# Performance work log

Measured on AMD Instinct MI355X. Metric: run time of the kernel, lower is better.

Reference implementation:

```python
import jax, jax.numpy as jnp
import numpy as np

H = 2048
Q_RANK = 256
SCALE = float(np.sqrt(Q_RANK))


def setup_inputs() -> dict:
    key = jax.random.key(0)
    k_x, k_s, k_a, k_o, k_b = jax.random.split(key, 5)
    B, L = 4, 4096
    x = jax.random.normal(k_x, (B, L, H), dtype=jnp.float32)
    # nn.Linear(H, q_rank, bias=False): weight [q_rank, H]; y = x @ W.T -> store transposed [H, q_rank]
    Ws = jax.random.normal(k_s, (H, Q_RANK), dtype=jnp.float32) / np.sqrt(H)
    Wa = jax.random.normal(k_a, (H, Q_RANK), dtype=jnp.float32) / np.sqrt(H)
    Wo = jax.random.normal(k_o, (H, H), dtype=jnp.float32) / np.sqrt(H)
    bo = jax.random.normal(k_b, (H,), dtype=jnp.float32) * 0.01
    return {"x": x, "Ws": Ws, "Wa": Wa, "Wo": Wo, "bo": bo}


def reference(x, Ws, Wa, Wo, bo):
    # x: [B, L, H]
    B, L, _ = x.shape
    state = jnp.einsum('blh,hr->blr', x, Ws)   # [B, L, r]
    action = jnp.einsum('blh,hr->blr', x, Wa)  # [B, L, r]
    q_values = jnp.einsum('bir,bjr->bij', state, action) / SCALE  # [B, L, L]
    # causal mask: position i attends to j <= i
    causal = jnp.tril(jnp.ones((L, L), dtype=bool))
    q_values = jnp.where(causal, q_values, -jnp.inf)
    weights = jax.nn.softmax(q_values, axis=-1)  # [B, L, L]
    out = jnp.einsum('bij,bjh->bih', weights, x)  # weights @ x (x acts as V)
    return jnp.einsum('bih,ho->bio', out, Wo.T) + bo  # out_proj: y = out @ Wo_lin.T; Wo stored as [H,H] input-major
```

## Files before the change

### kernel.cpp

```cpp
#include <hip/hip_runtime.h>
#include <hip/hip_bf16.h>
#include <cstdint>
#include <cstddef>
#include <cmath>

typedef __bf16 bf16_t;
typedef __bf16 bf16x8 __attribute__((ext_vector_type(8)));
typedef __bf16 bf16x4v __attribute__((ext_vector_type(4)));
typedef float f32x4 __attribute__((ext_vector_type(4)));

#define B_SZ 4
#define L_SZ 4096
#define H_SZ 2048
#define R_SZ 256
#define EXP_SC 0.090168440f
#define E2_ELEMS 8912896L
#define E2_BYTES 17825792L

#define GLDS16(gaddr, laddr)                                                    \
  __builtin_amdgcn_global_load_lds(                                             \
      (const __attribute__((address_space(1))) void*)(gaddr),                   \
      (__attribute__((address_space(3))) void*)(laddr), 16, 0, 0)

__device__ __forceinline__ f32x4 mfma16(bf16x8 a, bf16x8 b, f32x4 c) {
  return __builtin_amdgcn_mfma_f32_16x16x32_bf16(a, b, c, 0, 0, 0);
}

__device__ __forceinline__ float rsum16(float v) {
  v += __shfl_xor(v, 1, 16);
  v += __shfl_xor(v, 2, 16);
  v += __shfl_xor(v, 4, 16);
  v += __shfl_xor(v, 8, 16);
  return v;
}

__global__ void conv_kernel(const float* __restrict__ x, const float* __restrict__ Ws,
                            const float* __restrict__ Wa, const float* __restrict__ Wo,
                            bf16_t* __restrict__ xb, bf16_t* __restrict__ Wst,
                            bf16_t* __restrict__ Wat, bf16_t* __restrict__ Wob,
                            float* __restrict__ lsum) {
  const int bid = blockIdx.x;
  const int t = threadIdx.x;
  if (bid < 1280) {
    const int tid = bid * 256 + t;
    const int stride = 1280 * 256;
    const int n4 = B_SZ * L_SZ * H_SZ / 4;
    for (int i = tid; i < n4; i += stride) {
      float4 v = reinterpret_cast<const float4*>(x)[i];
      bf16x4v o;
      o[0] = (bf16_t)v.x; o[1] = (bf16_t)v.y; o[2] = (bf16_t)v.z; o[3] = (bf16_t)v.w;
      reinterpret_cast<bf16x4v*>(xb)[i] = o;
    }
  } else if (bid < 1920) {
    const int tid = (bid - 1280) * 256 + t;
    const int stride = 640 * 256;
    for (int idx = tid; idx < H_SZ * H_SZ / 4; idx += stride) {
      float4 v = reinterpret_cast<const float4*>(Wo)[idx];
      bf16x4v o;
      o[0] = (bf16_t)v.x; o[1] = (bf16_t)v.y; o[2] = (bf16_t)v.z; o[3] = (bf16_t)v.w;
      reinterpret_cast<bf16x4v*>(Wob)[idx] = o;
    }
  } else if (bid < 2040) {
    __shared__ float tile[32][33];
    const int j = t & 31;
    const int i4 = t >> 5;
    for (int tt = bid - 1920; tt < 1024; tt += 120) {
      const int mat = tt >> 9;
      const int ti = tt & 511;
      const int h0 = (ti >> 3) * 32;
      const int r0 = (ti & 7) * 32;
      const float* src = mat ? Wa : Ws;
      bf16_t* dst = mat ? Wat : Wst;
      __syncthreads();
#pragma unroll
      for (int p = 0; p < 4; ++p) {
        const int ii = p * 8 + i4;
        tile[ii][j] = src[(long)(h0 + ii) * R_SZ + r0 + j];
      }
      __syncthreads();
#pragma unroll
      for (int p = 0; p < 4; ++p) {
        const int rr = p * 8 + i4;
        dst[(long)(r0 + rr) * H_SZ + h0 + j] = (bf16_t)tile[j][rr];
      }
    }
  } else {
    const int tid = (bid - 2040) * 256 + t;
    const int stride = 8 * 256;
    for (int idx = tid; idx < B_SZ * L_SZ; idx += stride) lsum[idx] = 0.0f;
  }
}


#define G8_STG(P, REGION, BUFOFF, HALF)                                        \
  GLDS16((P)[0], lds + (REGION) + (BUFOFF) + (HALF)*16384 + ldst0);            \
  GLDS16((P)[1], lds + (REGION) + (BUFOFF) + (HALF)*16384 + ldst1);            \
  (P)[0] += 128; (P)[1] += 128;

#define G8_LDA(MH, BO) {                                                       \
  const char* ap_ = lds + (BO) + (MH)*16384;                                   \
  fa[0][0] = *(const bf16x8*)(ap_ + aOff0);                                    \
  fa[0][1] = *(const bf16x8*)(ap_ + aOff1);                                    \
  fa[1][0] = *(const bf16x8*)(ap_ + 4096 + aOff0);                             \
  fa[1][1] = *(const bf16x8*)(ap_ + 4096 + aOff1);                             \
  fa[2][0] = *(const bf16x8*)(ap_ + 8192 + aOff0);                             \
  fa[2][1] = *(const bf16x8*)(ap_ + 8192 + aOff1);                             \
  fa[3][0] = *(const bf16x8*)(ap_ + 12288 + aOff0);                            \
  fa[3][1] = *(const bf16x8*)(ap_ + 12288 + aOff1); }

#define G8_LDB(NH, BO) {                                                       \
  const char* bp_ = lds + 65536 + (BO) + (NH)*16384;                           \
  fb[NH][0][0] = *(const bf16x8*)(bp_ + bOff0);                                \
  fb[NH][0][1] = *(const bf16x8*)(bp_ + bOff1);                                \
  fb[NH][1][0] = *(const bf16x8*)(bp_ + 8192 + bOff0);                         \
  fb[NH][1][1] = *(const bf16x8*)(bp_ + 8192 + bOff1); }

#define G8_MM1(AM, AN, MF, NH, J)                                              \
  acc[AM][AN] = mfma16(fa[MF][1], fb[NH][J][1],                                \
                 mfma16(fa[MF][0], fb[NH][J][0], acc[AM][AN]))

#define G8_MM(MH, NH)                                                          \
  G8_MM1((MH)*4+0, (NH)*2+0, 0, NH, 0); G8_MM1((MH)*4+0, (NH)*2+1, 0, NH, 1); \
  G8_MM1((MH)*4+1, (NH)*2+0, 1, NH, 0); G8_MM1((MH)*4+1, (NH)*2+1, 1, NH, 1); \
  G8_MM1((MH)*4+2, (NH)*2+0, 2, NH, 0); G8_MM1((MH)*4+2, (NH)*2+1, 2, NH, 1); \
  G8_MM1((MH)*4+3, (NH)*2+0, 3, NH, 0); G8_MM1((MH)*4+3, (NH)*2+1, 3, NH, 1)

template <bool FULLN>
__device__ __forceinline__ void gemm8_core(
    const char* Ag, const char* Bg, long aRowB, long bRowB, int NT,
    char* lds, f32x4 (&acc)[8][4])
{
  const int t = threadIdx.x;
  const int l = t & 63;
  const int wid = t >> 6;
  const int wr = wid >> 2;
  const int wc = wid & 3;
  const int l15 = l & 15;
  const int l4 = l >> 4;
  const int swzm = (l15 & 7) << 4;
  const int aOff0 = (wr * 16 + l15) * 128 + ((l4 * 16) ^ swzm);
  const int aOff1 = (wr * 16 + l15) * 128 + ((64 + l4 * 16) ^ swzm);
  const int bOff0 = (wc * 16 + l15) * 128 + ((l4 * 16) ^ swzm);
  const int bOff1 = (wc * 16 + l15) * 128 + ((64 + l4 * 16) ^ swzm);
  const int d0 = t * 16, d1 = t * 16 + 8192;
  const int r0 = d0 >> 7, r1 = d1 >> 7;
  const int s0 = (d0 & 127) ^ ((r0 & 7) << 4);
  const int s1 = (d1 & 127) ^ ((r1 & 7) << 4);
  const char* pA0[2] = { Ag + (long)r0 * aRowB + s0, Ag + (long)r1 * aRowB + s1 };
  const char* pA1[2] = { Ag + (long)(128 + r0) * aRowB + s0, Ag + (long)(128 + r1) * aRowB + s1 };
  const char* pB0[2] = { Bg + (long)r0 * bRowB + s0, Bg + (long)r1 * bRowB + s1 };
  const char* pB1[2] = { Bg + (long)(128 + r0) * bRowB + s0, Bg + (long)(128 + r1) * bRowB + s1 };
  const int ldst0 = wid * 1024, ldst1 = wid * 1024 + 8192;
  bf16x8 fa[4][2], fb[2][2][2];

  G8_STG(pA0, 0, 0, 0);
  G8_STG(pB0, 65536, 0, 0);
  G8_STG(pA1, 0, 0, 1);
  if constexpr (FULLN) { G8_STG(pB1, 65536, 0, 1); }
  G8_STG(pA0, 0, 32768, 0);
  G8_STG(pB0, 65536, 32768, 0);
  asm volatile("s_waitcnt vmcnt(4)" ::: "memory");
  __builtin_amdgcn_sched_barrier(0);
  __builtin_amdgcn_s_barrier();

  int bufOff = 0;
  for (int T = 0; T < NT; ++T) {
    const int ob = bufOff ^ 32768;
    const bool stg1 = (T < NT - 1);
    const bool stg2 = (T < NT - 2);
    G8_LDA(0, bufOff);
    G8_LDB(0, bufOff);
    if constexpr (FULLN) { G8_LDB(1, bufOff); }
    if (stg1) {
      G8_STG(pA1, 0, ob, 1);
      if constexpr (FULLN) { G8_STG(pB1, 65536, ob, 1); }
    }
    __builtin_amdgcn_s_setprio(1);
    G8_MM(0, 0);
    if constexpr (FULLN) { G8_MM(0, 1); }
    __builtin_amdgcn_s_setprio(0);
    G8_LDA(1, bufOff);
    asm volatile("s_waitcnt lgkmcnt(8)" ::: "memory");
    __builtin_amdgcn_sched_barrier(0);
    __builtin_amdgcn_s_barrier();
    if (stg2) {
      G8_STG(pA0, 0, bufOff, 0);
      G8_STG(pB0, 65536, bufOff, 0);
    }
    asm volatile("s_waitcnt lgkmcnt(0)" ::: "memory");
    __builtin_amdgcn_s_setprio(1);
    G8_MM(1, 0);
    if constexpr (FULLN) { G8_MM(1, 1); }
    __builtin_amdgcn_s_setprio(0);
    if (stg2) {
      asm volatile("s_waitcnt vmcnt(4)" ::: "memory");
    } else if (stg1) {
      asm volatile("s_waitcnt vmcnt(0)" ::: "memory");
    }
    __builtin_amdgcn_sched_barrier(0);
    __builtin_amdgcn_s_barrier();
    bufOff ^= 32768;
  }
}

__global__ __launch_bounds__(512) void vq8_kernel(
    const bf16_t* __restrict__ Wob, const bf16_t* __restrict__ xb, bf16_t* __restrict__ VT,
    const bf16_t* __restrict__ Wst, const bf16_t* __restrict__ Wat,
    bf16_t* __restrict__ Qb, bf16_t* __restrict__ Kb)
{
  extern __shared__ char lds[];
  const int f = blockIdx.x;
  const int t = threadIdx.x, l = t & 63, wid = t >> 6;
  const int wr = wid >> 2, wc = wid & 3, l15 = l & 15, l4 = l >> 4;
  f32x4 acc[8][4] = {};
  if (f < 512) {
    const int lg = (f & 7) * 64 + (f >> 3);
    const int xo = lg & 7;
    const int yj = (lg >> 3) & 15;
    const int b  = lg >> 7;
    const long mBase = (long)xo * 256;
    const long nBase = (long)yj * 256;
    gemm8_core<true>((const char*)Wob + mBase * (H_SZ * 2),
                     (const char*)xb + ((long)b * L_SZ + nBase) * (H_SZ * 2),
                     H_SZ * 2, H_SZ * 2, H_SZ / 64, lds, acc);
    bf16_t* Cp = VT + (long)b * H_SZ * L_SZ;
#pragma unroll
    for (int am = 0; am < 8; ++am) {
#pragma unroll
      for (int an = 0; an < 4; ++an) {
        const long row = mBase + wr * 16 + am * 32 + l4 * 4;
        const long col = nBase + wc * 16 + an * 64 + l15;
#pragma unroll
        for (int r = 0; r < 4; ++r)
          Cp[(row + r) * L_SZ + col] = (bf16_t)acc[am][an][r];
      }
    }
  } else {
    const int qf = f - 512;
    const int lg = (qf & 7) * 32 + (qf >> 3);
    const int m = lg & 63;
    const int n = (lg >> 6) & 1;
    const int proj = lg >> 7;
    const long mBase = (long)m * 256;
    const long nBase = (long)n * 128;
    const bf16_t* W = proj ? Wat : Wst;
    bf16_t* Cp = proj ? Kb : Qb;
    gemm8_core<false>((const char*)xb + mBase * (H_SZ * 2),
                      (const char*)W + nBase * (H_SZ * 2),
                      H_SZ * 2, H_SZ * 2, H_SZ / 64, lds, acc);
#pragma unroll
    for (int am = 0; am < 8; ++am) {
#pragma unroll
      for (int an = 0; an < 2; ++an) {
        const long row = mBase + wr * 16 + am * 32 + l4 * 4;
        const long col = nBase + wc * 16 + an * 64 + l15;
#pragma unroll
        for (int r = 0; r < 4; ++r)
          Cp[(row + r) * R_SZ + col] = (bf16_t)acc[am][an][r];
      }
    }
  }
}

__global__ __launch_bounds__(512) void ep8_kernel(
    const bf16_t* __restrict__ Qb, const bf16_t* __restrict__ Kb,
    bf16_t* __restrict__ E, float* __restrict__ lsum)
{
  extern __shared__ char lds[];
  const int f = blockIdx.x;
  const int lg = (f & 7) * 68 + (f >> 3);
  const int b = lg / 136;
  const int t136 = lg - b * 136;
  int P = (int)((sqrtf((float)(8 * t136 + 1)) - 1.0f) * 0.5f);
  while ((P + 1) * (P + 2) / 2 <= t136) ++P;
  while (P * (P + 1) / 2 > t136) --P;
  const int Jp = t136 - P * (P + 1) / 2;

  f32x4 acc[8][4] = {};
  gemm8_core<true>((const char*)Qb + ((long)b * L_SZ + P * 256) * (R_SZ * 2),
                   (const char*)Kb + ((long)b * L_SZ + Jp * 256) * (R_SZ * 2),
                   R_SZ * 2, R_SZ * 2, R_SZ / 64, lds, acc);
  const int t = threadIdx.x, l = t & 63, wid = t >> 6;
  const int wr = wid >> 2, wc = wid & 3, l15 = l & 15, l4 = l >> 4;
  bf16_t* Ep = E + (long)b * E2_ELEMS + 32768L * P * (P + 1);
  const long ldaE = (long)(P + 1) * 256;
  float* lp = lsum + (long)b * L_SZ + P * 256;
  const bool diag = (Jp == P);
#pragma unroll
  for (int am = 0; am < 8; ++am) {
    const int rowi = wr * 16 + am * 32 + l4 * 4;
#pragma unroll
    for (int r = 0; r < 4; ++r) {
      float s = 0.0f;
#pragma unroll
      for (int an = 0; an < 4; ++an) {
        const int coli = wc * 16 + an * 64 + l15;
        float p = exp2f(acc[am][an][r] * EXP_SC);
        if (diag && coli > rowi + r) p = 0.0f;
        Ep[(long)(rowi + r) * ldaE + Jp * 256 + coli] = (bf16_t)p;
        s += p;
      }
      s = rsum16(s);
      if (l15 == 0) atomicAdd(lp + rowi + r, s);
    }
  }
}

__global__ __launch_bounds__(512) void pv8_kernel(
    const bf16_t* __restrict__ E, const bf16_t* __restrict__ VT,
    const float* __restrict__ lsum, const float* __restrict__ bo,
    float* __restrict__ out)
{
  extern __shared__ char lds[];
  const int f = blockIdx.x;
  const int lg = (f & 7) * 32 + (f >> 3);
  const int yj = lg & 7;
  const int pr = (lg >> 3) & 7;
  const int b  = lg >> 6;
  const int nBase = yj * 256;
  const int t = threadIdx.x, l = t & 63, wid = t >> 6;
  const int wr = wid >> 2, wc = wid & 3, l15 = l & 15, l4 = l >> 4;

#pragma unroll
  for (int s = 0; s < 2; ++s) {
    const int mt = s ? pr : (15 - pr);
    f32x4 acc[8][4] = {};
    const char* Ag = (const char*)E + (long)b * E2_BYTES + 65536L * mt * (mt + 1);
    const char* Bg = (const char*)VT + ((long)b * H_SZ + nBase) * (L_SZ * 2);
    gemm8_core<true>(Ag, Bg, (long)(mt + 1) * 512, L_SZ * 2, (mt + 1) * 4, lds, acc);
#pragma unroll
    for (int am = 0; am < 8; ++am) {
      const long rowG = (long)b * L_SZ + mt * 256 + wr * 16 + am * 32 + l4 * 4;
      float linv[4];
#pragma unroll
      for (int r = 0; r < 4; ++r) linv[r] = 1.0f / lsum[rowG + r];
#pragma unroll
      for (int an = 0; an < 4; ++an) {
        const int col = nBase + wc * 16 + an * 64 + l15;
        const float bias = bo[col];
#pragma unroll
        for (int r = 0; r < 4; ++r)
          out[(rowG + r) * H_SZ + col] = acc[am][an][r] * linv[r] + bias;
      }
    }
  }
}

extern "C" void kernel_launch(void* const* d_in, const int* in_sizes, int n_in,
                              void* d_out, int out_size, void* d_ws, size_t ws_size,
                              hipStream_t stream) {
  const float* x  = (const float*)d_in[0];
  const float* Ws = (const float*)d_in[1];
  const float* Wa = (const float*)d_in[2];
  const float* Wo = (const float*)d_in[3];
  const float* bo = (const float*)d_in[4];
  float* out = (float*)d_out;

  char* ws = (char*)d_ws;
  bf16_t* xb  = (bf16_t*)(ws + 0);
  bf16_t* Wst = (bf16_t*)(ws + 67108864);
  bf16_t* Wat = (bf16_t*)(ws + 68157440);
  bf16_t* Wob = (bf16_t*)(ws + 69206016);
  bf16_t* Qb  = (bf16_t*)(ws + 77594624);
  bf16_t* Kb  = (bf16_t*)(ws + 85983232);
  bf16_t* VT  = (bf16_t*)(ws + 94371840);
  float*  lsum = (float*)(ws + 161480704);
  bf16_t* E   = (bf16_t*)(ws + 0);

  hipFuncSetAttribute((const void*)vq8_kernel, hipFuncAttributeMaxDynamicSharedMemorySize, 131072);
  hipFuncSetAttribute((const void*)ep8_kernel, hipFuncAttributeMaxDynamicSharedMemorySize, 131072);
  hipFuncSetAttribute((const void*)pv8_kernel, hipFuncAttributeMaxDynamicSharedMemorySize, 131072);

  conv_kernel<<<dim3(2048), dim3(256), 0, stream>>>(x, Ws, Wa, Wo, xb, Wst, Wat, Wob, lsum);
  vq8_kernel<<<dim3(768), dim3(512), 131072, stream>>>(Wob, xb, VT, Wst, Wat, Qb, Kb);
  ep8_kernel<<<dim3(544), dim3(512), 131072, stream>>>(Qb, Kb, E, lsum);
  pv8_kernel<<<dim3(256), dim3(512), 131072, stream>>>(E, VT, lsum, bo, out);
}
```

Baseline: 367.5 us.

## Triple-buffer the B operand in LDS to prefetch two k-tiles ahead

The shared GEMM core now keeps the B tile in a ring of six 16KB LDS slots (three stages) instead of a double buffer, and issues B global-to-LDS loads two iterations ahead. The second B half (FULLN) is no longer staged just one iteration before use. vmcnt wait counts are adjusted to match, and the dynamic LDS allocation grows to 160KB for all three kernels. The aim is to hide more global-load latency for B, at the cost of using the full LDS budget and adding slot-rotation arithmetic.

Result: no change. 366.6 us (-0.2%).

```diff
diff --git a/kernel.cpp b/kernel.cpp
--- a/kernel.cpp
+++ b/kernel.cpp
@@ -16,6 +16,7 @@
 #define EXP_SC 0.090168440f
 #define E2_ELEMS 8912896L
 #define E2_BYTES 17825792L
+#define LDS_BYTES 163840
 
 #define GLDS16(gaddr, laddr)                                                    \
   __builtin_amdgcn_global_load_lds(                                             \
@@ -97,6 +98,11 @@
   GLDS16((P)[1], lds + (REGION) + (BUFOFF) + (HALF)*16384 + ldst1);            \
   (P)[0] += 128; (P)[1] += 128;
 
+#define GB_STG(P, S)                                                           \
+  GLDS16((P)[0], lds + 65536 + (S)*16384 + ldst0);                             \
+  GLDS16((P)[1], lds + 65536 + (S)*16384 + ldst1);                             \
+  (P)[0] += 128; (P)[1] += 128;
+
 #define G8_LDA(MH, BO) {                                                       \
   const char* ap_ = lds + (BO) + (MH)*16384;                                   \
   fa[0][0] = *(const bf16x8*)(ap_ + aOff0);                                    \
@@ -108,8 +114,8 @@
   fa[3][0] = *(const bf16x8*)(ap_ + 12288 + aOff0);                            \
   fa[3][1] = *(const bf16x8*)(ap_ + 12288 + aOff1); }
 
-#define G8_LDB(NH, BO) {                                                       \
-  const char* bp_ = lds + 65536 + (BO) + (NH)*16384;                           \
+#define G8_LDB(NH, S) {                                                        \
+  const char* bp_ = lds + 65536 + ((S) + (NH)) * 16384;                        \
   fb[NH][0][0] = *(const bf16x8*)(bp_ + bOff0);                                \
   fb[NH][0][1] = *(const bf16x8*)(bp_ + bOff1);                                \
   fb[NH][1][0] = *(const bf16x8*)(bp_ + 8192 + bOff0);                         \
@@ -154,26 +160,34 @@
   bf16x8 fa[4][2], fb[2][2][2];
 
   G8_STG(pA0, 0, 0, 0);
-  G8_STG(pB0, 65536, 0, 0);
   G8_STG(pA1, 0, 0, 1);
-  if constexpr (FULLN) { G8_STG(pB1, 65536, 0, 1); }
+  GB_STG(pB0, 0);
+  if constexpr (FULLN) { GB_STG(pB1, 1); }
   G8_STG(pA0, 0, 32768, 0);
-  G8_STG(pB0, 65536, 32768, 0);
-  asm volatile("s_waitcnt vmcnt(4)" ::: "memory");
+  GB_STG(pB0, 2);
+  if constexpr (FULLN) { GB_STG(pB1, 3); }
+  if constexpr (FULLN) {
+    asm volatile("s_waitcnt vmcnt(6)" ::: "memory");
+  } else {
+    asm volatile("s_waitcnt vmcnt(4)" ::: "memory");
+  }
   __builtin_amdgcn_sched_barrier(0);
   __builtin_amdgcn_s_barrier();
 
   int bufOff = 0;
+  int b0s = 0;
   for (int T = 0; T < NT; ++T) {
     const int ob = bufOff ^ 32768;
     const bool stg1 = (T < NT - 1);
     const bool stg2 = (T < NT - 2);
+    const int s4 = (b0s + 4 >= 6) ? (b0s - 2) : (b0s + 4);
     G8_LDA(0, bufOff);
-    G8_LDB(0, bufOff);
-    if constexpr (FULLN) { G8_LDB(1, bufOff); }
-    if (stg1) {
-      G8_STG(pA1, 0, ob, 1);
-      if constexpr (FULLN) { G8_STG(pB1, 65536, ob, 1); }
+    G8_LDB(0, b0s);
+    if constexpr (FULLN) { G8_LDB(1, b0s); }
+    if (stg1) { G8_STG(pA1, 0, ob, 1); }
+    if (stg2) {
+      GB_STG(pB0, s4);
+      if constexpr (FULLN) { GB_STG(pB1, s4 + 1); }
     }
     __builtin_amdgcn_s_setprio(1);
     G8_MM(0, 0);
@@ -183,23 +197,25 @@
     asm volatile("s_waitcnt lgkmcnt(8)" ::: "memory");
     __builtin_amdgcn_sched_barrier(0);
     __builtin_amdgcn_s_barrier();
-    if (stg2) {
-      G8_STG(pA0, 0, bufOff, 0);
-      G8_STG(pB0, 65536, bufOff, 0);
-    }
+    if (stg2) { G8_STG(pA0, 0, bufOff, 0); }
     asm volatile("s_waitcnt lgkmcnt(0)" ::: "memory");
     __builtin_amdgcn_s_setprio(1);
     G8_MM(1, 0);
     if constexpr (FULLN) { G8_MM(1, 1); }
     __builtin_amdgcn_s_setprio(0);
     if (stg2) {
-      asm volatile("s_waitcnt vmcnt(4)" ::: "memory");
+      if constexpr (FULLN) {
+        asm volatile("s_waitcnt vmcnt(6)" ::: "memory");
+      } else {
+        asm volatile("s_waitcnt vmcnt(4)" ::: "memory");
+      }
     } else if (stg1) {
       asm volatile("s_waitcnt vmcnt(0)" ::: "memory");
     }
     __builtin_amdgcn_sched_barrier(0);
     __builtin_amdgcn_s_barrier();
     bufOff ^= 32768;
+    b0s += 2; if (b0s >= 6) b0s -= 6;
   }
 }
 
@@ -367,12 +383,12 @@
   float*  lsum = (float*)(ws + 161480704);
   bf16_t* E   = (bf16_t*)(ws + 0);
 
-  hipFuncSetAttribute((const void*)vq8_kernel, hipFuncAttributeMaxDynamicSharedMemorySize, 131072);
-  hipFuncSetAttribute((const void*)ep8_kernel, hipFuncAttributeMaxDynamicSharedMemorySize, 131072);
-  hipFuncSetAttribute((const void*)pv8_kernel, hipFuncAttributeMaxDynamicSharedMemorySize, 131072);
+  hipFuncSetAttribute((const void*)vq8_kernel, hipFuncAttributeMaxDynamicSharedMemorySize, LDS_BYTES);
+  hipFuncSetAttribute((const void*)ep8_kernel, hipFuncAttributeMaxDynamicSharedMemorySize, LDS_BYTES);
+  hipFuncSetAttribute((const void*)pv8_kernel, hipFuncAttributeMaxDynamicSharedMemorySize, LDS_BYTES);
 
   conv_kernel<<<dim3(2048), dim3(256), 0, stream>>>(x, Ws, Wa, Wo, xb, Wst, Wat, Wob, lsum);
-  vq8_kernel<<<dim3(768), dim3(512), 131072, stream>>>(Wob, xb, VT, Wst, Wat, Qb, Kb);
-  ep8_kernel<<<dim3(544), dim3(512), 131072, stream>>>(Qb, Kb, E, lsum);
-  pv8_kernel<<<dim3(256), dim3(512), 131072, stream>>>(E, VT, lsum, bo, out);
-}
+  vq8_kernel<<<dim3(768), dim3(512), LDS_BYTES, stream>>>(Wob, xb, VT, Wst, Wat, Qb, Kb);
+  ep8_kernel<<<dim3(544), dim3(512), LDS_BYTES, stream>>>(Qb, Kb, E, lsum);
+  pv8_kernel<<<dim3(256), dim3(512), LDS_BYTES, stream>>>(E, VT, lsum, bo, out);
+}
```

## Restructure GEMM core into four barrier-separated MFMA phases with interleaved staging

Applied to the files above, without the earlier changes.

Splits the FULLN path of the shared GEMM core loop into four quadrant MFMA phases. Each phase is separated by workgroup barriers, and each global-to-LDS stage load is issued between phases so that memory traffic is spread across the tile iteration. The non-FULLN path is only reordered slightly. The goal is better overlap of LDS reads, global loads and MFMA work. The cost is more barriers per iteration and stricter lgkmcnt(0) waits, which may serialize work.

After: 375.9 us. 2.3% more time.

```diff
diff --git a/kernel.cpp b/kernel.cpp
--- a/kernel.cpp
+++ b/kernel.cpp
@@ -16,6 +16,7 @@
 #define EXP_SC 0.090168440f
 #define E2_ELEMS 8912896L
 #define E2_BYTES 17825792L
+#define LDS_BYTES 131072
 
 #define GLDS16(gaddr, laddr)                                                    \
   __builtin_amdgcn_global_load_lds(                                             \
@@ -124,6 +125,18 @@
   G8_MM1((MH)*4+1, (NH)*2+0, 1, NH, 0); G8_MM1((MH)*4+1, (NH)*2+1, 1, NH, 1); \
   G8_MM1((MH)*4+2, (NH)*2+0, 2, NH, 0); G8_MM1((MH)*4+2, (NH)*2+1, 2, NH, 1); \
   G8_MM1((MH)*4+3, (NH)*2+0, 3, NH, 0); G8_MM1((MH)*4+3, (NH)*2+1, 3, NH, 1)
+
+#define G8_BAR()                                                               \
+  __builtin_amdgcn_sched_barrier(0);                                           \
+  __builtin_amdgcn_s_barrier();
+
+#define G8_MFMA_PHASE(MH, NH)                                                  \
+  asm volatile("s_waitcnt lgkmcnt(0)" ::: "memory");                           \
+  __builtin_amdgcn_sched_barrier(0);                                           \
+  __builtin_amdgcn_s_setprio(1);                                               \
+  G8_MM(MH, NH);                                                               \
+  __builtin_amdgcn_s_setprio(0);                                               \
+  G8_BAR();
 
 template <bool FULLN>
 __device__ __forceinline__ void gemm8_core(
@@ -153,53 +166,86 @@
   const int ldst0 = wid * 1024, ldst1 = wid * 1024 + 8192;
   bf16x8 fa[4][2], fb[2][2][2];
 
-  G8_STG(pA0, 0, 0, 0);
-  G8_STG(pB0, 65536, 0, 0);
-  G8_STG(pA1, 0, 0, 1);
-  if constexpr (FULLN) { G8_STG(pB1, 65536, 0, 1); }
-  G8_STG(pA0, 0, 32768, 0);
-  G8_STG(pB0, 65536, 32768, 0);
-  asm volatile("s_waitcnt vmcnt(4)" ::: "memory");
-  __builtin_amdgcn_sched_barrier(0);
-  __builtin_amdgcn_s_barrier();
-
-  int bufOff = 0;
-  for (int T = 0; T < NT; ++T) {
-    const int ob = bufOff ^ 32768;
-    const bool stg1 = (T < NT - 1);
-    const bool stg2 = (T < NT - 2);
-    G8_LDA(0, bufOff);
-    G8_LDB(0, bufOff);
-    if constexpr (FULLN) { G8_LDB(1, bufOff); }
-    if (stg1) {
-      G8_STG(pA1, 0, ob, 1);
-      if constexpr (FULLN) { G8_STG(pB1, 65536, ob, 1); }
-    }
-    __builtin_amdgcn_s_setprio(1);
-    G8_MM(0, 0);
-    if constexpr (FULLN) { G8_MM(0, 1); }
-    __builtin_amdgcn_s_setprio(0);
-    G8_LDA(1, bufOff);
-    asm volatile("s_waitcnt lgkmcnt(8)" ::: "memory");
-    __builtin_amdgcn_sched_barrier(0);
-    __builtin_amdgcn_s_barrier();
-    if (stg2) {
-      G8_STG(pA0, 0, bufOff, 0);
-      G8_STG(pB0, 65536, bufOff, 0);
-    }
-    asm volatile("s_waitcnt lgkmcnt(0)" ::: "memory");
-    __builtin_amdgcn_s_setprio(1);
-    G8_MM(1, 0);
-    if constexpr (FULLN) { G8_MM(1, 1); }
-    __builtin_amdgcn_s_setprio(0);
-    if (stg2) {
-      asm volatile("s_waitcnt vmcnt(4)" ::: "memory");
-    } else if (stg1) {
-      asm volatile("s_waitcnt vmcnt(0)" ::: "memory");
-    }
-    __builtin_amdgcn_sched_barrier(0);
-    __builtin_amdgcn_s_barrier();
-    bufOff ^= 32768;
+  if constexpr (FULLN) {
+    G8_STG(pA0, 0, 0, 0);
+    G8_STG(pA1, 0, 0, 1);
+    G8_STG(pB0, 65536, 0, 0);
+    G8_STG(pB1, 65536, 0, 1);
+    G8_STG(pA0, 0, 32768, 0);
+    G8_STG(pB0, 65536, 32768, 0);
+    G8_STG(pA1, 0, 32768, 1);
+    asm volatile("s_waitcnt vmcnt(6)" ::: "memory");
+    G8_BAR();
+
+    int bufOff = 0;
+    for (int T = 0; T < NT; ++T) {
+      const int ob = bufOff ^ 32768;
+      const bool g1 = (T < NT - 1);
+      const bool g2 = (T < NT - 2);
+      G8_LDA(0, bufOff);
+      G8_LDB(0, bufOff);
+      if (g1) { G8_STG(pB1, 65536, ob, 1); }
+      asm volatile("s_waitcnt lgkmcnt(8)" ::: "memory");
+      G8_BAR();
+      G8_MFMA_PHASE(0, 0);
+      G8_LDB(1, bufOff);
+      if (g2) { G8_STG(pA0, 0, bufOff, 0); }
+      G8_BAR();
+      G8_MFMA_PHASE(0, 1);
+      G8_LDA(1, bufOff);
+      if (g2) { G8_STG(pB0, 65536, bufOff, 0); }
+      G8_BAR();
+      G8_MFMA_PHASE(1, 0);
+      if (g2) {
+        G8_STG(pA1, 0, bufOff, 1);
+        asm volatile("s_waitcnt vmcnt(6)" ::: "memory");
+      } else if (g1) {
+        asm volatile("s_waitcnt vmcnt(0)" ::: "memory");
+      }
+      G8_BAR();
+      __builtin_amdgcn_s_setprio(1);
+      G8_MM(1, 1);
+      __builtin_amdgcn_s_setprio(0);
+      G8_BAR();
+      bufOff = ob;
+    }
+  } else {
+    G8_STG(pA0, 0, 0, 0);
+    G8_STG(pA1, 0, 0, 1);
+    G8_STG(pB0, 65536, 0, 0);
+    G8_STG(pA0, 0, 32768, 0);
+    G8_STG(pB0, 65536, 32768, 0);
+    asm volatile("s_waitcnt vmcnt(4)" ::: "memory");
+    G8_BAR();
+
+    int bufOff = 0;
+    for (int T = 0; T < NT; ++T) {
+      const int ob = bufOff ^ 32768;
+      const bool g1 = (T < NT - 1);
+      const bool g2 = (T < NT - 2);
+      G8_LDA(0, bufOff);
+      G8_LDB(0, bufOff);
+      if (g1) { G8_STG(pA1, 0, ob, 1); }
+      __builtin_amdgcn_s_setprio(1);
+      G8_MM(0, 0);
+      __builtin_amdgcn_s_setprio(0);
+      G8_LDA(1, bufOff);
+      G8_BAR();
+      if (g2) {
+        G8_STG(pA0, 0, bufOff, 0);
+        G8_STG(pB0, 65536, bufOff, 0);
+      }
+      __builtin_amdgcn_s_setprio(1);
+      G8_MM(1, 0);
+      __builtin_amdgcn_s_setprio(0);
+      if (g2) {
+        asm volatile("s_waitcnt vmcnt(4)" ::: "memory");
+      } else if (g1) {
+        asm volatile("s_waitcnt vmcnt(0)" ::: "memory");
+      }
+      G8_BAR();
+      bufOff = ob;
+    }
   }
 }
 
@@ -367,12 +413,12 @@
   float*  lsum = (float*)(ws + 161480704);
   bf16_t* E   = (bf16_t*)(ws + 0);
 
-  hipFuncSetAttribute((const void*)vq8_kernel, hipFuncAttributeMaxDynamicSharedMemorySize, 131072);
-  hipFuncSetAttribute((const void*)ep8_kernel, hipFuncAttributeMaxDynamicSharedMemorySize, 131072);
-  hipFuncSetAttribute((const void*)pv8_kernel, hipFuncAttributeMaxDynamicSharedMemorySize, 131072);
+  hipFuncSetAttribute((const void*)vq8_kernel, hipFuncAttributeMaxDynamicSharedMemorySize, LDS_BYTES);
+  hipFuncSetAttribute((const void*)ep8_kernel, hipFuncAttributeMaxDynamicSharedMemorySize, LDS_BYTES);
+  hipFuncSetAttribute((const void*)pv8_kernel, hipFuncAttributeMaxDynamicSharedMemorySize, LDS_BYTES);
 
   conv_kernel<<<dim3(2048), dim3(256), 0, stream>>>(x, Ws, Wa, Wo, xb, Wst, Wat, Wob, lsum);
-  vq8_kernel<<<dim3(768), dim3(512), 131072, stream>>>(Wob, xb, VT, Wst, Wat, Qb, Kb);
-  ep8_kernel<<<dim3(544), dim3(512), 131072, stream>>>(Qb, Kb, E, lsum);
-  pv8_kernel<<<dim3(256), dim3(512), 131072, stream>>>(E, VT, lsum, bo, out);
-}
+  vq8_kernel<<<dim3(768), dim3(512), LDS_BYTES, stream>>>(Wob, xb, VT, Wst, Wat, Qb, Kb);
+  ep8_kernel<<<dim3(544), dim3(512), LDS_BYTES, stream>>>(Qb, Kb, E, lsum);
+  pv8_kernel<<<dim3(256), dim3(512), LDS_BYTES, stream>>>(E, VT, lsum, bo, out);
+}
```
